# Performance work log

Measured on AMD Instinct MI355X. Metric: run time of the kernel, lower is better.

## Reference

```python
import jax, jax.numpy as jnp
import numpy as np

N_NODES = 50000
N_EDGES = 800000
D_IN = 128
D_HID = 128
D_OUT = 2


def setup_inputs() -> dict:
    key = jax.random.key(0)
    ks = jax.random.split(key, 8)
    x = jax.random.normal(ks[0], (N_NODES, D_IN), dtype=jnp.float32)
    edge_index = jax.random.randint(ks[1], (2, N_EDGES), 0, N_NODES, dtype=jnp.int64)
    s = 0.05
    W1_l = jax.random.normal(ks[2], (D_HID, D_IN), dtype=jnp.float32) * s
    W1_r = jax.random.normal(ks[3], (D_HID, D_IN), dtype=jnp.float32) * s
    b1 = jax.random.normal(ks[4], (D_HID,), dtype=jnp.float32) * s
    W2_l = jax.random.normal(ks[5], (D_OUT, D_HID), dtype=jnp.float32) * s
    W2_r = jax.random.normal(ks[6], (D_OUT, D_HID), dtype=jnp.float32) * s
    b2 = jax.random.normal(ks[7], (D_OUT,), dtype=jnp.float32) * s
    return {"x": x, "edge_index": edge_index, "W1_l": W1_l, "W1_r": W1_r,
            "b1": b1, "W2_l": W2_l, "W2_r": W2_r, "b2": b2}


def _sage_conv(x, src, dst, W_l, W_r, b):
    # mean-aggregate neighbor features: gather from src, scatter-sum to dst
    n = x.shape[0]
    msg = x[src]                                            # [E, d]
    agg = jax.ops.segment_sum(msg, dst, num_segments=n)      # [n, d]
    cnt = jax.ops.segment_sum(jnp.ones((src.shape[0],), x.dtype), dst,
                              num_segments=n)
    agg = agg / jnp.maximum(cnt, 1.0)[:, None]
    # lin_l(aggregated) + lin_r(self) + bias  (PyG SAGEConv with root_weight)
    return agg @ W_l.T + x @ W_r.T + b


def reference(x, edge_index, W1_l, W1_r, b1, W2_l, W2_r, b2):
    src, dst = edge_index[0], edge_index[1]
    h = _sage_conv(x, src, dst, W1_l, W1_r, b1)
    h = jax.nn.relu(h)
    out = _sage_conv(h, src, dst, W2_l, W2_r, b2)
    return out
```

## Files before the change

### kernel.cpp

```cpp
#include <hip/hip_runtime.h>

#define N_NODES 50000
#define N_EDGES 800000

typedef __bf16 bf16_8 __attribute__((ext_vector_type(8)));
typedef float  f32_4  __attribute__((ext_vector_type(4)));


__global__ void prep_deg_kernel(const float* __restrict__ W1l, const float* __restrict__ W1r,
                                __bf16* __restrict__ Wt, const float* __restrict__ x,
                                __bf16* __restrict__ xb, const int* __restrict__ dst,
                                int* __restrict__ deg_p, int* __restrict__ edge_pos) {
    int b = blockIdx.x;
    if (b < 3125) {
        int t = b * 256 + threadIdx.x;
        int d = dst[t];
        int pos = atomicAdd(&deg_p[d * 16], 1);
        int node = t >> 4, c8 = t & 15;
        const float4* xp = (const float4*)(x + node * 128 + c8 * 8);
        float4 v0 = xp[0], v1 = xp[1];
        bf16_8 o;
        o[0] = (__bf16)v0.x; o[1] = (__bf16)v0.y; o[2] = (__bf16)v0.z; o[3] = (__bf16)v0.w;
        o[4] = (__bf16)v1.x; o[5] = (__bf16)v1.y; o[6] = (__bf16)v1.z; o[7] = (__bf16)v1.w;
        *(bf16_8*)(xb + t * 8) = o;
        edge_pos[t] = pos;
    } else {
        int t = (b - 3125) * 256 + threadIdx.x;
        int n = t >> 8, k = t & 255;
        float v = (k < 128) ? W1l[n * 128 + k] : W1r[n * 128 + (k - 128)];
        Wt[t] = (__bf16)v;
    }
}

__global__ void scan_block_kernel(const int* __restrict__ deg_p, int* __restrict__ rowptr,
                                  int* __restrict__ degc, int* __restrict__ bsum) {
    __shared__ int s[256];
    int i = blockIdx.x * 256 + threadIdx.x;
    int v = (i < N_NODES) ? deg_p[i * 16] : 0;
    if (i < N_NODES) degc[i] = v;
    s[threadIdx.x] = v;
    __syncthreads();
    #pragma unroll
    for (int off = 1; off < 256; off <<= 1) {
        int t = (threadIdx.x >= off) ? s[threadIdx.x - off] : 0;
        __syncthreads();
        s[threadIdx.x] += t;
        __syncthreads();
    }
    if (i < N_NODES) rowptr[i] = s[threadIdx.x] - v;
    if (threadIdx.x == 255) bsum[blockIdx.x] = s[255];
}

__device__ __forceinline__ void local_bsum_scan(const int* __restrict__ bsum,
                                                int* s_scan, int* s_boff) {
    int tid = threadIdx.x;
    int v = (tid < 196) ? bsum[tid] : 0;
    s_scan[tid] = v;
    __syncthreads();
    #pragma unroll
    for (int off = 1; off < 256; off <<= 1) {
        int t = (tid >= off) ? s_scan[tid - off] : 0;
        __syncthreads();
        s_scan[tid] += t;
        __syncthreads();
    }
    s_boff[tid] = s_scan[tid] - v;
    __syncthreads();
}

__global__ void fill_csr_kernel(const int* __restrict__ src, const int* __restrict__ dst,
                                const int* __restrict__ rowptr, const int* __restrict__ bsum,
                                const int* __restrict__ edge_pos, int* __restrict__ csr) {
    __shared__ int s_scan[256], s_boff[256];
    local_bsum_scan(bsum, s_scan, s_boff);
    int e = blockIdx.x * 256 + threadIdx.x;
    int d = dst[e];
    csr[rowptr[d] + s_boff[d >> 8] + edge_pos[e]] = src[e];
}

__global__ __launch_bounds__(256) void agg_kernel(
    const int* __restrict__ rowptr, const int* __restrict__ bsum,
    const int* __restrict__ degc, const int* __restrict__ csr,
    const __bf16* __restrict__ xb, __bf16* __restrict__ aggb)
{
    __shared__ int s_scan[256], s_boff[256];
    local_bsum_scan(bsum, s_scan, s_boff);
    int t = blockIdx.x * 256 + threadIdx.x;
    int node = t >> 4, c8 = t & 15;
    int beg = rowptr[node] + s_boff[node >> 8], n = degc[node];
    float acc[8] = {};
    int j = 0;
    for (; j + 4 <= n; j += 4) {
        int s0 = csr[beg + j],     s1 = csr[beg + j + 1];
        int s2 = csr[beg + j + 2], s3 = csr[beg + j + 3];
        bf16_8 v0 = *(const bf16_8*)(xb + s0 * 128 + c8 * 8);
        bf16_8 v1 = *(const bf16_8*)(xb + s1 * 128 + c8 * 8);
        bf16_8 v2 = *(const bf16_8*)(xb + s2 * 128 + c8 * 8);
        bf16_8 v3 = *(const bf16_8*)(xb + s3 * 128 + c8 * 8);
        #pragma unroll
        for (int u = 0; u < 8; ++u)
            acc[u] += ((float)v0[u] + (float)v1[u]) + ((float)v2[u] + (float)v3[u]);
    }
    for (; j < n; ++j) {
        int s0 = csr[beg + j];
        bf16_8 v0 = *(const bf16_8*)(xb + s0 * 128 + c8 * 8);
        #pragma unroll
        for (int u = 0; u < 8; ++u) acc[u] += (float)v0[u];
    }
    float inv = 1.0f / fmaxf((float)n, 1.0f);
    bf16_8 o;
    #pragma unroll
    for (int u = 0; u < 8; ++u) o[u] = (__bf16)(acc[u] * inv);
    *(bf16_8*)(aggb + t * 8) = o;
}

#define LDA 264
__global__ __launch_bounds__(256) void gemm_fused_kernel(
    const __bf16* __restrict__ aggb, const __bf16* __restrict__ xb,
    const __bf16* __restrict__ Wt, const float* __restrict__ b1,
    const float* __restrict__ W2l, const float* __restrict__ W2r,
    float* __restrict__ y, float* __restrict__ z)
{
    __shared__ __bf16 As[64 * LDA];
    const int i0 = blockIdx.x * 64;
    const int tid = threadIdx.x;

    #pragma unroll
    for (int s = 0; s < 8; ++s) {
        int v = tid + s * 256;
        int row = v >> 5, c8 = v & 31;
        int gi = i0 + row;
        bf16_8 val = {};
        if (gi < N_NODES) {
            val = (c8 < 16) ? *(const bf16_8*)(aggb + gi * 128 + c8 * 8)
                            : *(const bf16_8*)(xb + gi * 128 + (c8 - 16) * 8);
        }
        *(bf16_8*)(&As[row * LDA + c8 * 8]) = val;
    }
    __syncthreads();

    const int wv = tid >> 6, lane = tid & 63;
    const int m0 = wv * 16;
    const int mr = lane & 15, q = lane >> 4;

    f32_4 acc[8];
    #pragma unroll
    for (int nt = 0; nt < 8; ++nt) acc[nt] = (f32_4){0.f, 0.f, 0.f, 0.f};

    #pragma unroll
    for (int ks = 0; ks < 8; ++ks) {
        bf16_8 a = *(const bf16_8*)(&As[(m0 + mr) * LDA + ks * 32 + q * 8]);
        #pragma unroll
        for (int nt = 0; nt < 8; ++nt) {
            bf16_8 b = *(const bf16_8*)(Wt + (nt * 16 + mr) * 256 + ks * 32 + q * 8);
            acc[nt] = __builtin_amdgcn_mfma_f32_16x16x32_bf16(a, b, acc[nt], 0, 0, 0);
        }
    }

    float py0[4] = {}, py1[4] = {}, pz0[4] = {}, pz1[4] = {};
    #pragma unroll
    for (int nt = 0; nt < 8; ++nt) {
        int col = nt * 16 + mr;
        float bb  = b1[col];
        float wl0 = W2l[col], wl1 = W2l[128 + col];
        float wr0 = W2r[col], wr1 = W2r[128 + col];
        #pragma unroll
        for (int r = 0; r < 4; ++r) {
            float hv = fmaxf(acc[nt][r] + bb, 0.f);
            py0[r] += hv * wl0; py1[r] += hv * wl1;
            pz0[r] += hv * wr0; pz1[r] += hv * wr1;
        }
    }
    #pragma unroll
    for (int off = 1; off < 16; off <<= 1) {
        #pragma unroll
        for (int r = 0; r < 4; ++r) {
            py0[r] += __shfl_xor(py0[r], off);
            py1[r] += __shfl_xor(py1[r], off);
            pz0[r] += __shfl_xor(pz0[r], off);
            pz1[r] += __shfl_xor(pz1[r], off);
        }
    }
    if (mr < 4) {
        int r = mr;
        int row = i0 + m0 + q * 4 + r;
        if (row < N_NODES) {
            ((float2*)y)[row] = make_float2(py0[r], py1[r]);
            ((float2*)z)[row] = make_float2(pz0[r], pz1[r]);
        }
    }
}

__global__ void final_kernel(const int* __restrict__ rowptr, const int* __restrict__ bsum,
                             const int* __restrict__ degc, const int* __restrict__ csr,
                             const float* __restrict__ y, const float* __restrict__ z,
                             const float* __restrict__ b2, float* __restrict__ out) {
    __shared__ int s_scan[256], s_boff[256];
    local_bsum_scan(bsum, s_scan, s_boff);
    int t = blockIdx.x * 256 + threadIdx.x;
    if (t >= 2 * N_NODES) return;
    int node = t >> 1, c = t & 1;
    int beg = rowptr[node] + s_boff[node >> 8], n = degc[node];
    float acc = 0.f;
    for (int j = 0; j < n; ++j) acc += y[csr[beg + j] * 2 + c];
    out[t] = acc / fmaxf((float)n, 1.0f) + z[t] + b2[c];
}

extern "C" void kernel_launch(void* const* d_in, const int* in_sizes, int n_in,
                              void* d_out, int out_size, void* d_ws, size_t ws_size,
                              hipStream_t stream) {
    const float* x   = (const float*)d_in[0];
    const int*   ei  = (const int*)  d_in[1];
    const float* W1l = (const float*)d_in[2];
    const float* W1r = (const float*)d_in[3];
    const float* b1  = (const float*)d_in[4];
    const float* W2l = (const float*)d_in[5];
    const float* W2r = (const float*)d_in[6];
    const float* b2  = (const float*)d_in[7];
    float* out = (float*)d_out;
    const int* src = ei;
    const int* dst = ei + N_EDGES;

    char* ws = (char*)d_ws;
    int*    deg_p    = (int*)   (ws + 0);
    int*    edge_pos = (int*)   (ws + 3200000);
    int*    rowptr   = (int*)   (ws + 6400000);
    int*    degc     = (int*)   (ws + 6600192);
    int*    bsum     = (int*)   (ws + 6800384);
    int*    csr      = (int*)   (ws + 6801408);
    __bf16* xb       = (__bf16*)(ws + 10001408);
    __bf16* aggb     = (__bf16*)(ws + 22801408);
    float*  y        = (float*) (ws + 35601408);
    float*  z        = (float*) (ws + 36001408);
    __bf16* Wt       = (__bf16*)(ws + 36401408);

    hipMemsetAsync(deg_p, 0, 3200000, stream);
    prep_deg_kernel<<<3253, 256, 0, stream>>>(W1l, W1r, Wt, x, xb, dst, deg_p, edge_pos);
    scan_block_kernel<<<196, 256, 0, stream>>>(deg_p, rowptr, degc, bsum);
    fill_csr_kernel<<<3125, 256, 0, stream>>>(src, dst, rowptr, bsum, edge_pos, csr);
    agg_kernel<<<3125, 256, 0, stream>>>(rowptr, bsum, degc, csr, xb, aggb);
    gemm_fused_kernel<<<782, 256, 0, stream>>>(aggb, xb, Wt, b1, W2l, W2r, y, z);
    final_kernel<<<391, 256, 0, stream>>>(rowptr, bsum, degc, csr, y, z, b2, out);
}
```

Measured before the change: 211.2 us.

## Fuse neighbor aggregation into GEMM tile load and split final gather across lanes

Removes the separate aggregation kernel. The GEMM block now gathers and averages neighbor features for its 64 rows directly into shared memory, so the bf16 agg buffer is never written to or read back from global memory. The cost is a lower-occupancy GEMM kernel (64 rows per block, 782 blocks) doing latency-bound gathers, which cuts the parallelism available to hide gather latency. The final kernel now uses 4 lanes per node with float2 loads and shuffle reductions instead of one thread per output channel.

```diff
diff --git a/kernel.cpp b/kernel.cpp
--- a/kernel.cpp
+++ b/kernel.cpp
@@ -78,64 +78,65 @@
     csr[rowptr[d] + s_boff[d >> 8] + edge_pos[e]] = src[e];
 }
 
-__global__ __launch_bounds__(256) void agg_kernel(
+#define LDA 264
+__global__ __launch_bounds__(256) void gemm_fused_kernel(
     const int* __restrict__ rowptr, const int* __restrict__ bsum,
     const int* __restrict__ degc, const int* __restrict__ csr,
-    const __bf16* __restrict__ xb, __bf16* __restrict__ aggb)
+    const __bf16* __restrict__ xb, const __bf16* __restrict__ Wt,
+    const float* __restrict__ b1, const float* __restrict__ W2l,
+    const float* __restrict__ W2r, float* __restrict__ y, float* __restrict__ z)
 {
+    __shared__ __bf16 As[64 * LDA];
     __shared__ int s_scan[256], s_boff[256];
     local_bsum_scan(bsum, s_scan, s_boff);
-    int t = blockIdx.x * 256 + threadIdx.x;
-    int node = t >> 4, c8 = t & 15;
-    int beg = rowptr[node] + s_boff[node >> 8], n = degc[node];
-    float acc[8] = {};
-    int j = 0;
-    for (; j + 4 <= n; j += 4) {
-        int s0 = csr[beg + j],     s1 = csr[beg + j + 1];
-        int s2 = csr[beg + j + 2], s3 = csr[beg + j + 3];
-        bf16_8 v0 = *(const bf16_8*)(xb + s0 * 128 + c8 * 8);
-        bf16_8 v1 = *(const bf16_8*)(xb + s1 * 128 + c8 * 8);
-        bf16_8 v2 = *(const bf16_8*)(xb + s2 * 128 + c8 * 8);
-        bf16_8 v3 = *(const bf16_8*)(xb + s3 * 128 + c8 * 8);
-        #pragma unroll
-        for (int u = 0; u < 8; ++u)
-            acc[u] += ((float)v0[u] + (float)v1[u]) + ((float)v2[u] + (float)v3[u]);
-    }
-    for (; j < n; ++j) {
-        int s0 = csr[beg + j];
-        bf16_8 v0 = *(const bf16_8*)(xb + s0 * 128 + c8 * 8);
-        #pragma unroll
-        for (int u = 0; u < 8; ++u) acc[u] += (float)v0[u];
-    }
-    float inv = 1.0f / fmaxf((float)n, 1.0f);
-    bf16_8 o;
-    #pragma unroll
-    for (int u = 0; u < 8; ++u) o[u] = (__bf16)(acc[u] * inv);
-    *(bf16_8*)(aggb + t * 8) = o;
-}
-
-#define LDA 264
-__global__ __launch_bounds__(256) void gemm_fused_kernel(
-    const __bf16* __restrict__ aggb, const __bf16* __restrict__ xb,
-    const __bf16* __restrict__ Wt, const float* __restrict__ b1,
-    const float* __restrict__ W2l, const float* __restrict__ W2r,
-    float* __restrict__ y, float* __restrict__ z)
-{
-    __shared__ __bf16 As[64 * LDA];
+
     const int i0 = blockIdx.x * 64;
     const int tid = threadIdx.x;
 
     #pragma unroll
-    for (int s = 0; s < 8; ++s) {
+    for (int s = 0; s < 4; ++s) {
         int v = tid + s * 256;
-        int row = v >> 5, c8 = v & 31;
+        int row = v >> 4, c8 = v & 15;
         int gi = i0 + row;
         bf16_8 val = {};
+        if (gi < N_NODES) val = *(const bf16_8*)(xb + gi * 128 + c8 * 8);
+        *(bf16_8*)(&As[row * LDA + 128 + c8 * 8]) = val;
+    }
+
+    #pragma unroll
+    for (int s = 0; s < 4; ++s) {
+        int v = tid + s * 256;
+        int row = v >> 4, c8 = v & 15;
+        int gi = i0 + row;
+        float acc[8] = {};
+        int n = 0;
         if (gi < N_NODES) {
-            val = (c8 < 16) ? *(const bf16_8*)(aggb + gi * 128 + c8 * 8)
-                            : *(const bf16_8*)(xb + gi * 128 + (c8 - 16) * 8);
-        }
-        *(bf16_8*)(&As[row * LDA + c8 * 8]) = val;
+            int beg = rowptr[gi] + s_boff[gi >> 8];
+            n = degc[gi];
+            int j = 0;
+            for (; j + 4 <= n; j += 4) {
+                int s0 = csr[beg + j],     s1 = csr[beg + j + 1];
+                int s2 = csr[beg + j + 2], s3 = csr[beg + j + 3];
+                bf16_8 v0 = *(const bf16_8*)(xb + s0 * 128 + c8 * 8);
+                bf16_8 v1 = *(const bf16_8*)(xb + s1 * 128 + c8 * 8);
+                bf16_8 v2 = *(const bf16_8*)(xb + s2 * 128 + c8 * 8);
+                bf16_8 v3 = *(const bf16_8*)(xb + s3 * 128 + c8 * 8);
+                #pragma unroll
+                for (int u = 0; u < 8; ++u)
+                    acc[u] += ((float)v0[u] + (float)v1[u]) + ((float)v2[u] + (float)v3[u]);
+            }
+            for (; j < n; ++j) {
+                int s0 = csr[beg + j];
+                bf16_8 v0 = *(const bf16_8*)(xb + s0 * 128 + c8 * 8);
+                #pragma unroll
+                for (int u = 0; u < 8; ++u) acc[u] += (float)v0[u];
+            }
+        }
+        float inv = 1.0f / fmaxf((float)n, 1.0f);
+        bf16_8 o;
+        #pragma unroll
+        for (int u = 0; u < 8; ++u) o[u] = (__bf16)(acc[u] * inv);
+        *(bf16_8*)(&As[row * LDA + c8 * 8]) = o;
     }
     __syncthreads();
 
@@ -198,12 +199,22 @@
     __shared__ int s_scan[256], s_boff[256];
     local_bsum_scan(bsum, s_scan, s_boff);
     int t = blockIdx.x * 256 + threadIdx.x;
-    if (t >= 2 * N_NODES) return;
-    int node = t >> 1, c = t & 1;
+    int node = t >> 2, p = t & 3;
+    if (node >= N_NODES) return;
     int beg = rowptr[node] + s_boff[node >> 8], n = degc[node];
-    float acc = 0.f;
-    for (int j = 0; j < n; ++j) acc += y[csr[beg + j] * 2 + c];
-    out[t] = acc / fmaxf((float)n, 1.0f) + z[t] + b2[c];
+    float a0 = 0.f, a1 = 0.f;
+    for (int j = p; j < n; j += 4) {
+        float2 v = ((const float2*)y)[csr[beg + j]];
+        a0 += v.x; a1 += v.y;
+    }
+    a0 += __shfl_xor(a0, 1); a1 += __shfl_xor(a1, 1);
+    a0 += __shfl_xor(a0, 2); a1 += __shfl_xor(a1, 2);
+    if (p == 0) {
+        float inv = 1.0f / fmaxf((float)n, 1.0f);
+        float2 zz = ((const float2*)z)[node];
+        ((float2*)out)[node] = make_float2(a0 * inv + zz.x + b2[0],
+                                           a1 * inv + zz.y + b2[1]);
+    }
 }
 
 extern "C" void kernel_launch(void* const* d_in, const int* in_sizes, int n_in,
@@ -229,7 +240,6 @@
     int*    bsum     = (int*)   (ws + 6800384);
     int*    csr      = (int*)   (ws + 6801408);
     __bf16* xb       = (__bf16*)(ws + 10001408);
-    __bf16* aggb     = (__bf16*)(ws + 22801408);
     float*  y        = (float*) (ws + 35601408);
     float*  z        = (float*) (ws + 36001408);
     __bf16* Wt       = (__bf16*)(ws + 36401408);
@@ -238,7 +248,6 @@
     prep_deg_kernel<<<3253, 256, 0, stream>>>(W1l, W1r, Wt, x, xb, dst, deg_p, edge_pos);
     scan_block_kernel<<<196, 256, 0, stream>>>(deg_p, rowptr, degc, bsum);
     fill_csr_kernel<<<3125, 256, 0, stream>>>(src, dst, rowptr, bsum, edge_pos, csr);
-    agg_kernel<<<3125, 256, 0, stream>>>(rowptr, bsum, degc, csr, xb, aggb);
-    gemm_fused_kernel<<<782, 256, 0, stream>>>(aggb, xb, Wt, b1, W2l, W2r, y, z);
-    final_kernel<<<391, 256, 0, stream>>>(rowptr, bsum, degc, csr, y, z, b2, out);
-}
+    gemm_fused_kernel<<<782, 256, 0, stream>>>(rowptr, bsum, degc, csr, xb, Wt, b1, W2l, W2r, y, z);
+    final_kernel<<<782, 256, 0, stream>>>(rowptr, bsum, degc, csr, y, z, b2, out);
+}
```

After: 223.7 us. 1.06x slower.
